# Performance work log

Hardware: AMD Instinct MI355X
Metric: run time of the kernel (lower is better)

## Reference

```python
import jax, jax.numpy as jnp
import numpy as np
from jax import lax

NUM_CLASSES = 2
NUM_PROTO = 10
C = 720


def _conv(x, w, b, pad):
    # x: [B,Cin,H,W], w: [Cout,Cin,kh,kw]
    y = lax.conv_general_dilated(x, w, (1, 1), ((pad, pad), (pad, pad)),
                                 dimension_numbers=('NCHW', 'OIHW', 'NCHW'))
    return y + b[None, :, None, None]


def _bn(x, g, b, rm, rv):
    inv = g / jnp.sqrt(rv + 1e-5)
    return (x - rm[None, :, None, None]) * inv[None, :, None, None] + b[None, :, None, None]


def _ln(x, g, b):
    mu = jnp.mean(x, -1, keepdims=True)
    var = jnp.var(x, -1, keepdims=True)
    return (x - mu) / jnp.sqrt(var + 1e-5) * g + b


def _l2n(x):
    n = jnp.linalg.norm(x, axis=-1, keepdims=True)
    return x / jnp.maximum(n, 1e-12)


def _resize_bilinear_ac(x, oh, ow):
    # bilinear with align_corners=True, x: [B,C,H,W]
    B, Cc, H, W = x.shape
    ys = jnp.linspace(0.0, H - 1.0, oh)
    xs = jnp.linspace(0.0, W - 1.0, ow)
    y0 = jnp.floor(ys).astype(jnp.int32)
    y1 = jnp.minimum(y0 + 1, H - 1)
    wy = (ys - y0).astype(x.dtype)
    x0 = jnp.floor(xs).astype(jnp.int32)
    x1 = jnp.minimum(x0 + 1, W - 1)
    wx = (xs - x0).astype(x.dtype)
    r = x[:, :, y0, :] * (1 - wy)[None, None, :, None] + x[:, :, y1, :] * wy[None, None, :, None]
    return r[:, :, :, x0] * (1 - wx) + r[:, :, :, x1] * wx


def setup_inputs() -> dict:
    key = jax.random.key(0)
    ks = jax.random.split(key, 8)
    B, H = 2, 96
    f32 = jnp.float32
    return {
        'feat1': jax.random.normal(ks[0], (B, 48, H, H), f32),
        'feat2': jax.random.normal(ks[1], (B, 96, H // 2, H // 2), f32),
        'feat3': jax.random.normal(ks[2], (B, 192, H // 4, H // 4), f32),
        'feat4': jax.random.normal(ks[3], (B, 384, H // 8, H // 8), f32),
        'cls_w': jax.random.normal(ks[4], (C, C, 3, 3), f32) * 0.02,
        'cls_b': jnp.zeros((C,), f32),
        'cls_bn_g': jnp.ones((C,), f32),
        'cls_bn_b': jnp.zeros((C,), f32),
        'cls_bn_rm': jnp.zeros((C,), f32),
        'cls_bn_rv': jnp.ones((C,), f32),
        'proj_w1': jax.random.normal(ks[5], (C, C, 1, 1), f32) * 0.02,
        'proj_b1': jnp.zeros((C,), f32),
        'proj_bn_g': jnp.ones((C,), f32),
        'proj_bn_b': jnp.zeros((C,), f32),
        'proj_bn_rm': jnp.zeros((C,), f32),
        'proj_bn_rv': jnp.ones((C,), f32),
        'proj_w2': jax.random.normal(ks[6], (C, C, 1, 1), f32) * 0.02,
        'proj_b2': jnp.zeros((C,), f32),
        'ln_feat_g': jnp.ones((C,), f32),
        'ln_feat_b': jnp.zeros((C,), f32),
        'ln_mask_g': jnp.ones((NUM_CLASSES,), f32),
        'ln_mask_b': jnp.zeros((NUM_CLASSES,), f32),
        'prototypes': jax.random.normal(ks[7], (NUM_CLASSES, NUM_PROTO, C), f32) * 0.02,
    }


def reference(feat1, feat2, feat3, feat4, cls_w, cls_b, cls_bn_g, cls_bn_b, cls_bn_rm,
              cls_bn_rv, proj_w1, proj_b1, proj_bn_g, proj_bn_b, proj_bn_rm, proj_bn_rv,
              proj_w2, proj_b2, ln_feat_g, ln_feat_b, ln_mask_g, ln_mask_b, prototypes):
    B, _, h, w = feat1.shape
    feats = jnp.concatenate([
        feat1,
        _resize_bilinear_ac(feat2, h, w),
        _resize_bilinear_ac(feat3, h, w),
        _resize_bilinear_ac(feat4, h, w),
    ], axis=1)  # [B,720,h,w]
    # cls_head: Conv3x3 + BN + ReLU (Dropout2d is identity in eval)
    c = jax.nn.relu(_bn(_conv(feats, cls_w, cls_b, 1), cls_bn_g, cls_bn_b, cls_bn_rm, cls_bn_rv))
    # proj_head (convmlp): Conv1x1 + BN + ReLU + Conv1x1
    p = jax.nn.relu(_bn(_conv(c, proj_w1, proj_b1, 0), proj_bn_g, proj_bn_b, proj_bn_rm, proj_bn_rv))
    p = _conv(p, proj_w2, proj_b2, 0)
    # (b h w) c
    _c = p.transpose(0, 2, 3, 1).reshape(-1, C)
    _c = _l2n(_ln(_c, ln_feat_g, ln_feat_b))
    protos = _l2n(prototypes)  # [K,M,C]
    masks = jnp.einsum('nd,kmd->nmk', _c, protos)  # [N,M,K]
    out_seg = jnp.max(masks, axis=1)               # [N,K]
    out_seg = _ln(out_seg, ln_mask_g, ln_mask_b)
    out_seg = out_seg.reshape(B, h, w, NUM_CLASSES).transpose(0, 3, 1, 2)
    return out_seg
```

## Files before the change

kernel.cpp:

```cpp
#include <hip/hip_runtime.h>
#include <float.h>

#define WDIM 96
#define HW   9216
#define PH   98
#define IMG  (PH*PH)
#define NPIXP (2*IMG)
#define NPIX 19328
#define GUARD 128
#define GPIX (NPIX + 2*GUARD)
#define NKG_ACT 96
#define MDIM 768
#define G3 824
#define G1 104

typedef _Float16 f16;
typedef f16  f16x8 __attribute__((ext_vector_type(8)));
typedef f16  f16x4 __attribute__((ext_vector_type(4)));
typedef float f32x4 __attribute__((ext_vector_type(4)));
typedef unsigned int u32;

typedef __attribute__((address_space(1))) const u32 gu32;
typedef __attribute__((address_space(3))) u32 lu32;
__device__ __forceinline__ void gld16(const f16* g, f16* s)
{
    __builtin_amdgcn_global_load_lds((gu32*)g, (lu32*)s, 16, 0, 0);
}

__global__ void prep_kernel(
    const float* __restrict__ cls_b,
    const float* __restrict__ g0, const float* __restrict__ b0,
    const float* __restrict__ rm0, const float* __restrict__ rv0,
    const float* __restrict__ p1b,
    const float* __restrict__ g1, const float* __restrict__ b1,
    const float* __restrict__ rm1, const float* __restrict__ rv1,
    const float* __restrict__ p2b,
    const float* __restrict__ protos,
    float* __restrict__ alpha, float* __restrict__ beta,
    float* __restrict__ protoN)
{
    __shared__ float red[4];
    if (blockIdx.x == 0) {
        for (int i = threadIdx.x; i < MDIM; i += blockDim.x) {
            if (i < 720) {
                float s0 = g0[i] * rsqrtf(rv0[i] + 1e-5f);
                alpha[i] = s0;
                beta[i]  = (cls_b[i] - rm0[i]) * s0 + b0[i];
                float s1 = g1[i] * rsqrtf(rv1[i] + 1e-5f);
                alpha[MDIM + i] = s1;
                beta[MDIM + i]  = (p1b[i] - rm1[i]) * s1 + b1[i];
                alpha[2*MDIM + i] = 1.0f;
                beta[2*MDIM + i]  = p2b[i];
            } else {
                alpha[i] = 0.f; beta[i] = 0.f;
                alpha[MDIM + i] = 0.f; beta[MDIM + i] = 0.f;
                alpha[2*MDIM + i] = 0.f; beta[2*MDIM + i] = 0.f;
            }
        }
    } else {
        int row = blockIdx.x - 1;
        const float* src = protos + row * 720;
        float s = 0.f;
        for (int i = threadIdx.x; i < 720; i += blockDim.x) { float v = src[i]; s += v * v; }
        #pragma unroll
        for (int off = 32; off > 0; off >>= 1) s += __shfl_down(s, off);
        int wave = threadIdx.x >> 6, lane = threadIdx.x & 63;
        if (lane == 0) red[wave] = s;
        __syncthreads();
        float tot = red[0] + red[1] + red[2] + red[3];
        float rn = 1.0f / fmaxf(sqrtf(tot), 1e-12f);
        for (int i = threadIdx.x; i < 720; i += blockDim.x)
            protoN[row * 720 + i] = src[i] * rn;
    }
}

__global__ __launch_bounds__(256)
void w3trans_kernel(const float* __restrict__ w3,
                    f16* __restrict__ W3h, f16* __restrict__ W3l)
{
    int tid = blockIdx.x * blockDim.x + threadIdx.x;
    int kgl = tid / MDIM;
    int o   = tid - kgl * MDIM;
    if (kgl > 90) return;

    if (kgl == 90) {
        f16x8 z = {0, 0, 0, 0, 0, 0, 0, 0};
        for (int g = 810; g < G3; ++g) {
            size_t off = ((size_t)g * MDIM + o) * 8;
            *(f16x8*)(W3h + off) = z;
            *(f16x8*)(W3l + off) = z;
        }
        return;
    }

    float buf[72];
    if (o < 720) {
        const float* src = w3 + (size_t)o * 6480 + kgl * 72;
        #pragma unroll
        for (int c = 0; c < 72; ++c) buf[c] = src[c];
    } else {
        #pragma unroll
        for (int c = 0; c < 72; ++c) buf[c] = 0.f;
    }

    #pragma unroll
    for (int s = 0; s < 9; ++s) {
        f16x8 hv, lv;
        #pragma unroll
        for (int c = 0; c < 8; ++c) {
            float v = buf[c * 9 + s];
            f16 h = (f16)v;
            hv[c] = h;
            lv[c] = (f16)(v - (float)h);
        }
        size_t off = ((size_t)(kgl * 9 + s) * MDIM + o) * 8;
        *(f16x8*)(W3h + off) = hv;
        *(f16x8*)(W3l + off) = lv;
    }
}

__global__ void w1trans_kernel(const float* __restrict__ w1a,
                               const float* __restrict__ w1b,
                               f16* __restrict__ W1ah, f16* __restrict__ W1al,
                               f16* __restrict__ W1bh, f16* __restrict__ W1bl)
{
    int tid = blockIdx.x * blockDim.x + threadIdx.x;
    const int N1 = G1 * MDIM;
    const float* src; f16 *dh, *dl; int g, o;
    if (tid < N1)            { g = tid / MDIM; o = tid - g * MDIM; src = w1a; dh = W1ah; dl = W1al; }
    else if (tid < 2 * N1)   { int u = tid - N1; g = u / MDIM; o = u - g * MDIM; src = w1b; dh = W1bh; dl = W1bl; }
    else return;

    float v[8];
    #pragma unroll
    for (int j = 0; j < 8; ++j) v[j] = 0.f;
    if (g < 90 && o < 720) {
        #pragma unroll
        for (int j = 0; j < 8; ++j)
            v[j] = src[(size_t)o * 720 + g * 8 + j];
    }
    f16x8 hv, lv;
    #pragma unroll
    for (int j = 0; j < 8; ++j) {
        f16 h = (f16)v[j];
        hv[j] = h;
        lv[j] = (f16)(v[j] - (float)h);
    }
    size_t off = ((size_t)g * MDIM + o) * 8;
    *(f16x8*)(dh + off) = hv;
    *(f16x8*)(dl + off) = lv;
}

__global__ void upsample_kernel(const float* __restrict__ f1,
                                const float* __restrict__ f2,
                                const float* __restrict__ f3,
                                const float* __restrict__ f4,
                                f16* __restrict__ Xhi, f16* __restrict__ Xlo)
{
    int tid = blockIdx.x * blockDim.x + threadIdx.x;
    if (tid >= 90 * GPIX) return;
    int kg = tid / GPIX;
    int gp = tid - kg * GPIX;
    int p  = gp - GUARD;
    float v[8];
    #pragma unroll
    for (int j = 0; j < 8; ++j) v[j] = 0.f;
    if (p >= 0 && p < NPIXP) {
        int b = p / IMG; int rem = p - b * IMG;
        int y = rem / PH; int x = rem - y * PH;
        if (y >= 1 && y <= 96 && x >= 1 && x <= 96) {
            int oy = y - 1, ox = x - 1;
            int c0 = kg * 8;
            if (c0 < 48) {
                #pragma unroll
                for (int j = 0; j < 8; ++j)
                    v[j] = f1[((size_t)(b * 48 + c0 + j)) * HW + oy * 96 + ox];
            } else {
                const float* src; int Cs, Hs, cb;
                if (c0 < 144)      { src = f2; Cs = 96;  Hs = 48; cb = c0 - 48; }
                else if (c0 < 336) { src = f3; Cs = 192; Hs = 24; cb = c0 - 144; }
                else               { src = f4; Cs = 384; Hs = 12; cb = c0 - 336; }
                float scale = (float)(Hs - 1) / 95.0f;
                float yf = oy * scale, xf = ox * scale;
                int y0 = (int)yf, x0 = (int)xf;
                float wy = yf - y0, wx = xf - x0;
                int y1 = min(y0 + 1, Hs - 1), x1 = min(x0 + 1, Hs - 1);
                #pragma unroll
                for (int j = 0; j < 8; ++j) {
                    const float* sb = src + (size_t)(b * Cs + cb + j) * Hs * Hs;
                    float v00 = sb[y0 * Hs + x0], v01 = sb[y0 * Hs + x1];
                    float v10 = sb[y1 * Hs + x0], v11 = sb[y1 * Hs + x1];
                    float r0 = v00 * (1.f - wy) + v10 * wy;
                    float r1 = v01 * (1.f - wy) + v11 * wy;
                    v[j] = r0 * (1.f - wx) + r1 * wx;
                }
            }
        }
    }
    f16x8 hv, lv;
    #pragma unroll
    for (int j = 0; j < 8; ++j) {
        f16 h = (f16)v[j];
        hv[j] = h;
        lv[j] = (f16)(v[j] - (float)h);
    }
    size_t off = (size_t)tid * 8;
    *(f16x8*)(Xhi + off) = hv;
    *(f16x8*)(Xlo + off) = lv;
}

template<int NSTEP, int CONV3>
__global__ __launch_bounds__(256, 2)
void mfma_gemm(const f16* __restrict__ Whi, const f16* __restrict__ Wlo,
               const f16* __restrict__ Bhi_, const f16* __restrict__ Blo_,
               f16* __restrict__ Ohi, f16* __restrict__ Olo,
               const float* __restrict__ alpha, const float* __restrict__ beta,
               int relu)
{
    __shared__ f16 sA[2][4][2][128][8];
    __shared__ f16 sB[2][4][2][128][8];

    const int l = blockIdx.x;
    const int xcd = l & 7;
    const int j0 = l >> 3;
    const int ncol = xcd * 19 + j0 / 6;
    if (ncol >= 151) return;
    const int m0 = (j0 % 6) * 128;
    const int n0 = ncol * 128;

    const int t = threadIdx.x;
    const int lane = t & 63;
    const int wid = __builtin_amdgcn_readfirstlane(t >> 6);
    const int wm = wid >> 1, wn = wid & 1;
    const int quad = lane >> 4, ln = lane & 15;
    const int loff = lane * 8;

    f32x4 acc[4][4];
    #pragma unroll
    for (int i = 0; i < 4; ++i)
        #pragma unroll
        for (int j = 0; j < 4; ++j)
            acc[i][j] = (f32x4){0.f, 0.f, 0.f, 0.f};

    const f16* aHu = Whi + ((size_t)wid * MDIM + m0) * 8;
    const f16* aLu = Wlo + ((size_t)wid * MDIM + m0) * 8;
    const size_t aAdv = (size_t)4 * MDIM * 8;

    auto stage = [&](int st, int slot) {
        const f16* ah = aHu + (size_t)st * aAdv;
        const f16* al = aLu + (size_t)st * aAdv;
        f16* dA = &sA[slot][wid][0][0][0];
        gld16(ah + loff,        dA);
        gld16(ah + 512 + loff,  dA + 512);
        gld16(al + loff,        dA + 1024);
        gld16(al + 512 + loff,  dA + 1536);
        const int g = 4 * st + wid;
        long long brow;
        if (CONV3) {
            int gc = g > 809 ? 809 : g;
            int kgl = gc / 9;
            int s2 = gc - kgl * 9;
            brow = (long long)kgl * GPIX + (s2 / 3 - 1) * PH + (s2 % 3 - 1);
        } else {
            int gc = g > 89 ? 89 : g;
            brow = (long long)gc * GPIX;
        }
        const f16* bh = Bhi_ + (brow + n0) * 8;
        const f16* bl = Blo_ + (brow + n0) * 8;
        f16* dB = &sB[slot][wid][0][0][0];
        gld16(bh + loff,        dB);
        gld16(bh + 512 + loff,  dB + 512);
        gld16(bl + loff,        dB + 1024);
        gld16(bl + 512 + loff,  dB + 1536);
    };

    auto read_frags = [&](f16x8 (&a)[8], f16x8 (&b)[8], int c) {
        #pragma unroll
        for (int mt = 0; mt < 4; ++mt) {
            a[mt]     = *(const f16x8*)&sA[c][quad][0][wm * 64 + mt * 16 + ln][0];
            a[mt + 4] = *(const f16x8*)&sA[c][quad][1][wm * 64 + mt * 16 + ln][0];
            b[mt]     = *(const f16x8*)&sB[c][quad][0][wn * 64 + mt * 16 + ln][0];
            b[mt + 4] = *(const f16x8*)&sB[c][quad][1][wn * 64 + mt * 16 + ln][0];
        }
    };

    auto compute = [&](f16x8 (&av)[8], f16x8 (&bv)[8]) {
        #pragma unroll
        for (int mt = 0; mt < 4; ++mt)
            #pragma unroll
            for (int nt = 0; nt < 4; ++nt)
                acc[mt][nt] = __builtin_amdgcn_mfma_f32_16x16x32_f16(av[mt], bv[nt], acc[mt][nt], 0, 0, 0);
        #pragma unroll
        for (int mt = 0; mt < 4; ++mt)
            #pragma unroll
            for (int nt = 0; nt < 4; ++nt)
                acc[mt][nt] = __builtin_amdgcn_mfma_f32_16x16x32_f16(av[mt], bv[nt + 4], acc[mt][nt], 0, 0, 0);
        #pragma unroll
        for (int mt = 0; mt < 4; ++mt)
            #pragma unroll
            for (int nt = 0; nt < 4; ++nt)
                acc[mt][nt] = __builtin_amdgcn_mfma_f32_16x16x32_f16(av[mt + 4], bv[nt], acc[mt][nt], 0, 0, 0);
    };

    f16x8 aP[8], bP[8], aQ[8], bQ[8];

#define BODY(S, SS, PA, PB, QA, QB)                                   \
    do {                                                              \
        stage((S) + 2, (SS));                                         \
        asm volatile("s_waitcnt vmcnt(8)" ::: "memory");              \
        __builtin_amdgcn_s_barrier();                                 \
        read_frags(QA, QB, (SS) ^ 1);                                 \
        __builtin_amdgcn_sched_barrier(0);                            \
        __builtin_amdgcn_s_setprio(1);                                \
        compute(PA, PB);                                              \
        __builtin_amdgcn_s_setprio(0);                                \
        asm volatile("s_waitcnt lgkmcnt(0)" ::: "memory");            \
        __builtin_amdgcn_sched_barrier(0);                            \
        __builtin_amdgcn_s_barrier();                                 \
    } while (0)

    stage(0, 0);
    stage(1, 1);
    asm volatile("s_waitcnt vmcnt(8)" ::: "memory");
    __builtin_amdgcn_s_barrier();
    read_frags(aP, bP, 0);
    asm volatile("s_waitcnt lgkmcnt(0)" ::: "memory");
    __builtin_amdgcn_sched_barrier(0);
    __builtin_amdgcn_s_barrier();

    int s = 0;
    #pragma unroll 1
    for (; s + 1 < NSTEP; s += 2) {
        BODY(s,     0, aP, bP, aQ, bQ);
        BODY(s + 1, 1, aQ, bQ, aP, bP);
    }
    if (s < NSTEP)
        BODY(s, 0, aP, bP, aQ, bQ);
#undef BODY

    #pragma unroll
    for (int mt = 0; mt < 4; ++mt) {
        const int rowb = m0 + wm * 64 + mt * 16 + quad * 4;
        const float4 a4 = *(const float4*)(alpha + rowb);
        const float4 b4 = *(const float4*)(beta + rowb);
        const size_t kg = rowb >> 3;
        const int sub = rowb & 7;
        #pragma unroll
        for (int nt = 0; nt < 4; ++nt) {
            const int P = n0 + wn * 64 + nt * 16 + ln;
            float v0 = acc[mt][nt][0] * a4.x + b4.x;
            float v1 = acc[mt][nt][1] * a4.y + b4.y;
            float v2 = acc[mt][nt][2] * a4.z + b4.z;
            float v3 = acc[mt][nt][3] * a4.w + b4.w;
            if (relu) {
                v0 = fmaxf(v0, 0.f); v1 = fmaxf(v1, 0.f);
                v2 = fmaxf(v2, 0.f); v3 = fmaxf(v3, 0.f);
            }
            f16 h0 = (f16)v0, h1 = (f16)v1, h2 = (f16)v2, h3 = (f16)v3;
            f16x4 hv = {h0, h1, h2, h3};
            f16x4 lv = {(f16)(v0 - (float)h0), (f16)(v1 - (float)h1),
                        (f16)(v2 - (float)h2), (f16)(v3 - (float)h3)};
            size_t o = (kg * GPIX + P) * 8 + sub;
            *(f16x4*)(Ohi + o) = hv;
            *(f16x4*)(Olo + o) = lv;
        }
    }
}

__global__ __launch_bounds__(256)
void head_kernel(const f16* __restrict__ Yhi, const f16* __restrict__ Ylo,
                 const float* __restrict__ lng, const float* __restrict__ lnb,
                 const float* __restrict__ protoN,
                 const float* __restrict__ lmg, const float* __restrict__ lmb,
                 float* __restrict__ out)
{
    const int t = threadIdx.x;
    const int wv = t >> 6, lane = t & 63;
    const int pw = lane >> 4, sub = lane & 15;
    const int p = blockIdx.x * 16 + wv * 4 + pw;
    const int b = p / HW; const int r = p - b * HW;
    const int y = r / 96; const int x = r - y * 96;
    const size_t P = (size_t)b * IMG + (y + 1) * PH + (x + 1);

    f16x8 xh[6], xl[6];
    float s1 = 0.f, s2 = 0.f;
    #pragma unroll
    for (int k = 0; k < 6; ++k) {
        int kg = sub + 16 * k;
        if (kg < 90) {
            xh[k] = *(const f16x8*)(Yhi + ((size_t)kg * GPIX + P) * 8);
            xl[k] = *(const f16x8*)(Ylo + ((size_t)kg * GPIX + P) * 8);
            #pragma unroll
            for (int j = 0; j < 8; ++j) {
                float v = (float)xh[k][j] + (float)xl[k][j];
                s1 += v; s2 += v * v;
            }
        }
    }
    #pragma unroll
    for (int m = 1; m < 16; m <<= 1) {
        s1 += __shfl_xor(s1, m);
        s2 += __shfl_xor(s2, m);
    }
    float mu  = s1 * (1.0f / 720.0f);
    float var = s2 * (1.0f / 720.0f) - mu * mu;
    float inv = rsqrtf(var + 1e-5f);

    float dots[20];
    #pragma unroll
    for (int q = 0; q < 20; ++q) dots[q] = 0.f;
    float nrm = 0.f;
    #pragma unroll
    for (int k = 0; k < 6; ++k) {
        int kg = sub + 16 * k;
        if (kg < 90) {
            const int c0 = kg * 8;
            #pragma unroll
            for (int j = 0; j < 8; ++j) {
                const int c = c0 + j;
                float v = ((float)xh[k][j] + (float)xl[k][j] - mu) * inv * lng[c] + lnb[c];
                nrm += v * v;
                #pragma unroll
                for (int q = 0; q < 20; ++q)
                    dots[q] = fmaf(v, protoN[q * 720 + c], dots[q]);
            }
        }
    }
    #pragma unroll
    for (int m = 1; m < 16; m <<= 1) {
        nrm += __shfl_xor(nrm, m);
        #pragma unroll
        for (int q = 0; q < 20; ++q) dots[q] += __shfl_xor(dots[q], m);
    }

    if (sub == 0) {
        float rn = 1.0f / fmaxf(sqrtf(nrm), 1e-12f);
        float m0v = -FLT_MAX, m1v = -FLT_MAX;
        #pragma unroll
        for (int q = 0; q < 10; ++q) m0v = fmaxf(m0v, dots[q]);
        #pragma unroll
        for (int q = 10; q < 20; ++q) m1v = fmaxf(m1v, dots[q]);
        m0v *= rn; m1v *= rn;
        float mu2 = 0.5f * (m0v + m1v);
        float dv  = m0v - mu2;
        float va  = dv * dv;
        float iv  = rsqrtf(va + 1e-5f);
        float o0 = (m0v - mu2) * iv * lmg[0] + lmb[0];
        float o1 = (m1v - mu2) * iv * lmg[1] + lmb[1];
        out[b * (2 * HW) + r]      = o0;
        out[b * (2 * HW) + HW + r] = o1;
    }
}

extern "C" void kernel_launch(void* const* d_in, const int* in_sizes, int n_in,
                              void* d_out, int out_size, void* d_ws, size_t ws_size,
                              hipStream_t stream)
{
    const float* feat1      = (const float*)d_in[0];
    const float* feat2      = (const float*)d_in[1];
    const float* feat3      = (const float*)d_in[2];
    const float* feat4      = (const float*)d_in[3];
    const float* cls_w      = (const float*)d_in[4];
    const float* cls_b      = (const float*)d_in[5];
    const float* cls_bn_g   = (const float*)d_in[6];
    const float* cls_bn_b   = (const float*)d_in[7];
    const float* cls_bn_rm  = (const float*)d_in[8];
    const float* cls_bn_rv  = (const float*)d_in[9];
    const float* proj_w1    = (const float*)d_in[10];
    const float* proj_b1    = (const float*)d_in[11];
    const float* proj_bn_g  = (const float*)d_in[12];
    const float* proj_bn_b  = (const float*)d_in[13];
    const float* proj_bn_rm = (const float*)d_in[14];
    const float* proj_bn_rv = (const float*)d_in[15];
    const float* proj_w2    = (const float*)d_in[16];
    const float* proj_b2    = (const float*)d_in[17];
    const float* ln_feat_g  = (const float*)d_in[18];
    const float* ln_feat_b  = (const float*)d_in[19];
    const float* ln_mask_g  = (const float*)d_in[20];
    const float* ln_mask_b  = (const float*)d_in[21];
    const float* protos     = (const float*)d_in[22];

    const size_t PLANEH = (size_t)NKG_ACT * GPIX * 8;
    const size_t W3SZ   = (size_t)G3 * MDIM * 8;
    const size_t W1SZ   = (size_t)G1 * MDIM * 8;

    f16* Xhi  = (f16*)d_ws;
    f16* Xlo  = Xhi + PLANEH;
    f16* Yhi  = Xlo + PLANEH;
    f16* Ylo  = Yhi + PLANEH;
    f16* W3h  = Ylo + PLANEH;
    f16* W3l  = W3h + W3SZ;
    f16* W1ah = W3l + W3SZ;
    f16* W1al = W1ah + W1SZ;
    f16* W1bh = W1al + W1SZ;
    f16* W1bl = W1bh + W1SZ;
    float* alphas = (float*)(W1bl + W1SZ);
    float* betas  = alphas + 3 * MDIM;
    float* protoN = betas + 3 * MDIM;

    prep_kernel<<<21, 256, 0, stream>>>(cls_b, cls_bn_g, cls_bn_b, cls_bn_rm, cls_bn_rv,
                                        proj_b1, proj_bn_g, proj_bn_b, proj_bn_rm, proj_bn_rv,
                                        proj_b2, protos, alphas, betas, protoN);
    {
        int total = 91 * MDIM;
        w3trans_kernel<<<(total + 255) / 256, 256, 0, stream>>>(cls_w, W3h, W3l);
    }
    {
        int total = 2 * G1 * MDIM;
        w1trans_kernel<<<(total + 255) / 256, 256, 0, stream>>>(proj_w1, proj_w2,
                                                                W1ah, W1al, W1bh, W1bl);
    }
    {
        int total = 90 * GPIX;
        upsample_kernel<<<(total + 255) / 256, 256, 0, stream>>>(feat1, feat2, feat3, feat4,
                                                                 Xhi, Xlo);
    }

    const size_t GOFF = (size_t)GUARD * 8;
    const int NBLK = 912;
    mfma_gemm<203, 1><<<NBLK, 256, 0, stream>>>(W3h, W3l, Xhi + GOFF, Xlo + GOFF,
                                                Yhi + GOFF, Ylo + GOFF,
                                                alphas, betas, 1);
    mfma_gemm<23, 0><<<NBLK, 256, 0, stream>>>(W1ah, W1al, Yhi + GOFF, Ylo + GOFF,
                                               Xhi + GOFF, Xlo + GOFF,
                                               alphas + MDIM, betas + MDIM, 1);
    mfma_gemm<23, 0><<<NBLK, 256, 0, stream>>>(W1bh, W1bl, Xhi + GOFF, Xlo + GOFF,
                                               Yhi + GOFF, Ylo + GOFF,
                                               alphas + 2 * MDIM, betas + 2 * MDIM, 0);

    head_kernel<<<HW * 2 / 16, 256, 0, stream>>>(Yhi + GOFF, Ylo + GOFF,
                                                 ln_feat_g, ln_feat_b, protoN,
                                                 ln_mask_g, ln_mask_b, (float*)d_out);
}
```

Measured before the change: 746.3 us.

## Load weight fragments directly from global into registers, bypassing LDS

New measurement: 707.2 us, median of 3. 1.06x faster.

```diff
diff --git a/kernel.cpp b/kernel.cpp
--- a/kernel.cpp
+++ b/kernel.cpp
@@ -217,7 +217,6 @@
                const float* __restrict__ alpha, const float* __restrict__ beta,
                int relu)
 {
-    __shared__ f16 sA[2][4][2][128][8];
     __shared__ f16 sB[2][4][2][128][8];
 
     const int l = blockIdx.x;
@@ -242,18 +241,10 @@
         for (int j = 0; j < 4; ++j)
             acc[i][j] = (f32x4){0.f, 0.f, 0.f, 0.f};
 
-    const f16* aHu = Whi + ((size_t)wid * MDIM + m0) * 8;
-    const f16* aLu = Wlo + ((size_t)wid * MDIM + m0) * 8;
-    const size_t aAdv = (size_t)4 * MDIM * 8;
-
-    auto stage = [&](int st, int slot) {
-        const f16* ah = aHu + (size_t)st * aAdv;
-        const f16* al = aLu + (size_t)st * aAdv;
-        f16* dA = &sA[slot][wid][0][0][0];
-        gld16(ah + loff,        dA);
-        gld16(ah + 512 + loff,  dA + 512);
-        gld16(al + loff,        dA + 1024);
-        gld16(al + 512 + loff,  dA + 1536);
+    const size_t aLane = ((size_t)quad * MDIM + m0 + wm * 64 + ln) * 8;
+    const size_t aAdv  = (size_t)4 * MDIM * 8;
+
+    auto stage_B = [&](int st, int slot) {
         const int g = 4 * st + wid;
         long long brow;
         if (CONV3) {
@@ -274,11 +265,19 @@
         gld16(bl + 512 + loff,  dB + 1536);
     };
 
-    auto read_frags = [&](f16x8 (&a)[8], f16x8 (&b)[8], int c) {
+    auto load_A = [&](f16x8 (&a)[8], int st) {
+        const f16* ah = Whi + aLane + (size_t)st * aAdv;
+        const f16* al = Wlo + aLane + (size_t)st * aAdv;
         #pragma unroll
         for (int mt = 0; mt < 4; ++mt) {
-            a[mt]     = *(const f16x8*)&sA[c][quad][0][wm * 64 + mt * 16 + ln][0];
-            a[mt + 4] = *(const f16x8*)&sA[c][quad][1][wm * 64 + mt * 16 + ln][0];
+            a[mt]     = *(const f16x8*)(ah + mt * 128);
+            a[mt + 4] = *(const f16x8*)(al + mt * 128);
+        }
+    };
+
+    auto read_B = [&](f16x8 (&b)[8], int c) {
+        #pragma unroll
+        for (int mt = 0; mt < 4; ++mt) {
             b[mt]     = *(const f16x8*)&sB[c][quad][0][wn * 64 + mt * 16 + ln][0];
             b[mt + 4] = *(const f16x8*)&sB[c][quad][1][wn * 64 + mt * 16 + ln][0];
         }
@@ -302,14 +301,16 @@
                 acc[mt][nt] = __builtin_amdgcn_mfma_f32_16x16x32_f16(av[mt + 4], bv[nt], acc[mt][nt], 0, 0, 0);
     };
 
-    f16x8 aP[8], bP[8], aQ[8], bQ[8];
+    f16x8 aP[8], aQ[8], bP[8], bQ[8];
 
 #define BODY(S, SS, PA, PB, QA, QB)                                   \
     do {                                                              \
-        stage((S) + 2, (SS));                                         \
-        asm volatile("s_waitcnt vmcnt(8)" ::: "memory");              \
+        stage_B((S) + 2, (SS));                                       \
+        load_A(QA, (S) + 1);                                          \
+        __builtin_amdgcn_sched_barrier(0);                            \
+        asm volatile("s_waitcnt vmcnt(20)" ::: "memory");             \
         __builtin_amdgcn_s_barrier();                                 \
-        read_frags(QA, QB, (SS) ^ 1);                                 \
+        read_B(QB, (SS) ^ 1);                                         \
         __builtin_amdgcn_sched_barrier(0);                            \
         __builtin_amdgcn_s_setprio(1);                                \
         compute(PA, PB);                                              \
@@ -319,11 +320,13 @@
         __builtin_amdgcn_s_barrier();                                 \
     } while (0)
 
-    stage(0, 0);
-    stage(1, 1);
-    asm volatile("s_waitcnt vmcnt(8)" ::: "memory");
+    stage_B(0, 0);
+    stage_B(1, 1);
+    load_A(aP, 0);
+    __builtin_amdgcn_sched_barrier(0);
+    asm volatile("s_waitcnt vmcnt(12)" ::: "memory");
     __builtin_amdgcn_s_barrier();
-    read_frags(aP, bP, 0);
+    read_B(bP, 0);
     asm volatile("s_waitcnt lgkmcnt(0)" ::: "memory");
     __builtin_amdgcn_sched_barrier(0);
     __builtin_amdgcn_s_barrier();
```
